# Kernel tuning notes

Measured on AMD Instinct MI355X. Metric: run time of the kernel, lower is better.

## Reference

```python
import jax, jax.numpy as jnp
import numpy as np

B, D_IN, NQ, H = 65536, 385, 64, 16  # batch, input dim, num questions, head width
DIMS = [385, 512, 256, 192]


def setup_inputs() -> dict:
    key = jax.random.key(0)
    ks = jax.random.split(key, 12)
    s = 0.02
    inp = {
        "x": jax.random.normal(ks[0], (B, D_IN), jnp.float32),
        "W1": jax.random.normal(ks[1], (DIMS[0], DIMS[1]), jnp.float32) * s,
        "b1": jnp.zeros((DIMS[1],), jnp.float32),
        "W2": jax.random.normal(ks[2], (DIMS[1], DIMS[2]), jnp.float32) * s,
        "b2": jnp.zeros((DIMS[2],), jnp.float32),
        "W3": jax.random.normal(ks[3], (DIMS[2], DIMS[3]), jnp.float32) * s,
        "b3": jnp.zeros((DIMS[3],), jnp.float32),
        # all true/false heads stacked: layout [qid, correct, H] flattened on last axis
        "Wh": jax.random.normal(ks[4], (DIMS[3], NQ * 2 * H), jnp.float32) * s,
        "bh": jnp.zeros((NQ * 2 * H,), jnp.float32),
        "question_ids": jax.random.randint(ks[5], (B,), 0, NQ, jnp.int32),
        "is_correct": jax.random.randint(ks[6], (B,), 0, 2, jnp.int32),
    }
    return inp


def reference(x, W1, b1, W2, b2, W3, b3, Wh, bh, question_ids, is_correct):
    # shared trunk (dropout is identity at eval); activation = relu
    h = jax.nn.relu(x @ W1 + b1)          # [B, 512]
    h = jax.nn.relu(h @ W2 + b2)          # [B, 256]
    h = jax.nn.relu(h @ W3 + b3)          # [B, 192] shared features
    # compute all heads densely, then gather the per-row head slice —
    # equivalent to routing each row to its (question_id, is_correct) Linear head
    logits_all = h @ Wh + bh              # [B, NQ*2*H]
    base = (question_ids * 2 + is_correct) * H        # [B]
    idx = base[:, None] + jnp.arange(H)[None, :]      # [B, H]
    return jnp.take_along_axis(logits_all, idx, axis=1)  # [B, H]
```

## Files before the change

### kernel.cpp

```cpp
#include <hip/hip_runtime.h>
#include <hip/hip_bf16.h>

#define THREADS 512
#define ROWS 64

typedef __attribute__((ext_vector_type(4))) float f32x4;
typedef __attribute__((ext_vector_type(8))) short s16x8;

__device__ __forceinline__ unsigned short bfbits(float f) {
  __bf16 h = (__bf16)f;
  return __builtin_bit_cast(unsigned short, h);
}
__device__ __forceinline__ float bf2f(unsigned short h) {
  unsigned u = ((unsigned)h) << 16;
  return __builtin_bit_cast(float, u);
}

__global__ void prep_kernel(const float* __restrict__ W1, const float* __restrict__ W2,
                            const float* __restrict__ W3, const float* __restrict__ Wh,
                            unsigned short* __restrict__ w1f, unsigned short* __restrict__ w2f,
                            unsigned short* __restrict__ w3f, unsigned short* __restrict__ whT) {
  int u = blockIdx.x * blockDim.x + threadIdx.x;
  const int U1 = 24576, U2 = 16384, U3 = 6144, U4 = 49152;
  if (u < U1) {
    int lane = u & 63, r = (u >> 6) & 31, c = u >> 11;
    int f  = r * 16 + (lane & 15);
    int kb = c * 32 + ((lane >> 4) << 3);
    s16x8 v;
    #pragma unroll
    for (int j = 0; j < 8; ++j) v[j] = (short)bfbits(W1[(kb + j) * 512 + f]);
    *(s16x8*)(w1f + (u << 3)) = v;
    return;
  }
  u -= U1;
  if (u < U2) {
    int lane = u & 63, r = (u >> 6) & 15, c = u >> 10;
    int f  = r * 16 + (lane & 15);
    int kb = c * 32 + ((lane >> 4) << 3);
    s16x8 v;
    #pragma unroll
    for (int j = 0; j < 8; ++j) v[j] = (short)bfbits(W2[(kb + j) * 256 + f]);
    *(s16x8*)(w2f + (u << 3)) = v;
    return;
  }
  u -= U2;
  if (u < U3) {
    int lane = u & 63, t = u >> 6;
    int c = t / 12, r = t - c * 12;
    int f  = r * 16 + (lane & 15);
    int kb = c * 32 + ((lane >> 4) << 3);
    s16x8 v;
    #pragma unroll
    for (int j = 0; j < 8; ++j) v[j] = (short)bfbits(W3[(kb + j) * 192 + f]);
    *(s16x8*)(w3f + (u << 3)) = v;
    return;
  }
  u -= U3;
  if (u < U4) {
    int j = u & 15, v2 = u >> 4;
    int fo = v2 % 24, head = v2 / 24;
    s16x8 v;
    #pragma unroll
    for (int i = 0; i < 8; ++i) v[i] = (short)bfbits(Wh[(fo * 8 + i) * 2048 + head * 16 + j]);
    *(s16x8*)(whT + u * 8) = v;
  }
}

#define MFMA(a, b, c) __builtin_amdgcn_mfma_f32_16x16x32_bf16((a), (b), (c), 0, 0, 0)
#define SWZ(lp) (((lp) * 16) ^ ((((lp) >> 4) & 3) << 5))

#define G1_RANGE(P, C0, C1)                                                                 \
  _Pragma("unroll")                                                                         \
  for (int c = (C0); c < (C1); ++c) {                                                       \
    s16x8 a0 = *(const s16x8*)(w1f + (((c * 32 + (P) * 16 + w * 2 + 0) * 64 + lane) << 3)); \
    s16x8 a1 = *(const s16x8*)(w1f + (((c * 32 + (P) * 16 + w * 2 + 1) * 64 + lane) << 3)); \
    _Pragma("unroll")                                                                       \
    for (int bt = 0; bt < 4; ++bt) {                                                        \
      s16x8 bfr = *(const s16x8*)(xall + (c << 12) + (bt << 10) + swz_l);                   \
      acc1[0][bt] = MFMA(a0, bfr, acc1[0][bt]);                                             \
      acc1[1][bt] = MFMA(a1, bfr, acc1[1][bt]);                                             \
    }                                                                                       \
  }

__global__ __launch_bounds__(THREADS, 4)
void fused_mlp(const float* __restrict__ x,
               const float* __restrict__ b1,
               const float* __restrict__ b2,
               const float* __restrict__ b3,
               const float* __restrict__ bh,
               const float* __restrict__ W1,
               const int* __restrict__ qid,
               const int* __restrict__ corr,
               const unsigned short* __restrict__ w1f,
               const unsigned short* __restrict__ w2f,
               const unsigned short* __restrict__ w3f,
               const unsigned short* __restrict__ whT,
               float* __restrict__ out) {
  __shared__ __align__(16) unsigned char lds[81920];
  unsigned char*  xall = lds;
  unsigned char*  h1L  = lds;
  unsigned short* h3b  = (unsigned short*)lds;
  unsigned char*  h1H  = lds + 49152;
  unsigned char*  h2f  = lds + 49152;

  const int tid  = threadIdx.x;
  const int lane = tid & 63;
  const int w    = tid >> 6;
  const int b0   = blockIdx.x * ROWS;
  const int l15  = lane & 15;
  const int lh   = lane >> 4;
  const int swz_l = SWZ(lane);

  const int s_ci = tid >> 8;
  const int s_wi = tid & 255;
  const int s_bt = s_wi >> 6;
  const int s_lp = s_wi & 63;
  const float* s_base = x + (size_t)(b0 + (s_bt << 4) + (s_lp & 15)) * 385 + ((s_lp >> 4) << 3);
  const int s_abase = (s_bt << 10) + SWZ(s_lp);

  f32x4 sv0, sv1;
  auto sload = [&](int g) {
    int c = (g << 1) + s_ci;
    sv0 = *(const f32x4*)(s_base + c * 32);
    sv1 = *(const f32x4*)(s_base + c * 32 + 4);
  };
  auto swrite = [&](int g) {
    int c = (g << 1) + s_ci;
    s16x8 v;
    v[0] = (short)bfbits(sv0[0]); v[1] = (short)bfbits(sv0[1]);
    v[2] = (short)bfbits(sv0[2]); v[3] = (short)bfbits(sv0[3]);
    v[4] = (short)bfbits(sv1[0]); v[5] = (short)bfbits(sv1[1]);
    v[6] = (short)bfbits(sv1[2]); v[7] = (short)bfbits(sv1[3]);
    *(s16x8*)(xall + (c << 12) + s_abase) = v;
  };

  f32x4 acc1[2][4];
  #pragma unroll
  for (int a = 0; a < 2; ++a)
    #pragma unroll
    for (int bt = 0; bt < 4; ++bt) acc1[a][bt] = (f32x4)0.0f;

  auto epi1 = [&](int P, unsigned char* dst) {
    #pragma unroll
    for (int a = 0; a < 2; ++a) {
      int ft = w * 2 + a;
      int fg = P * 256 + (ft << 4) + (lh << 2);
      f32x4 bv = *(const f32x4*)(b1 + fg);
      f32x4 wv = *(const f32x4*)(W1 + 384 * 512 + fg);
      int so = ((ft >> 1) << 12) + SWZ(l15 + ((((ft & 1) << 1) + (lh >> 1)) << 4)) + ((lh & 1) << 3);
      #pragma unroll
      for (int bt = 0; bt < 4; ++bt) {
        float xv = x[(size_t)(b0 + (bt << 4) + l15) * 385 + 384];
        float v0 = fmaxf(acc1[a][bt][0] + bv[0] + wv[0] * xv, 0.f);
        float v1 = fmaxf(acc1[a][bt][1] + bv[1] + wv[1] * xv, 0.f);
        float v2 = fmaxf(acc1[a][bt][2] + bv[2] + wv[2] * xv, 0.f);
        float v3 = fmaxf(acc1[a][bt][3] + bv[3] + wv[3] * xv, 0.f);
        unsigned plo = (unsigned)bfbits(v0) | ((unsigned)bfbits(v1) << 16);
        unsigned phi = (unsigned)bfbits(v2) | ((unsigned)bfbits(v3) << 16);
        unsigned long long pk = (unsigned long long)plo | ((unsigned long long)phi << 32);
        *(unsigned long long*)(dst + so + (bt << 10)) = pk;
        acc1[a][bt] = (f32x4)0.0f;
      }
    }
  };

  sload(0); swrite(0);
  __syncthreads();

  sload(1); G1_RANGE(0, 0, 2)  swrite(1); __syncthreads();
  sload(2); G1_RANGE(0, 2, 4)  swrite(2); __syncthreads();
  sload(3); G1_RANGE(0, 4, 6)  swrite(3); __syncthreads();
  sload(4); G1_RANGE(0, 6, 8)  swrite(4); __syncthreads();
  sload(5); G1_RANGE(0, 8, 10) swrite(5); __syncthreads();

  G1_RANGE(0, 10, 12)
  epi1(0, h1H);

  G1_RANGE(1, 0, 12)
  __syncthreads();
  epi1(1, h1L);
  __syncthreads();

  f32x4 acc2[2][4];
  #pragma unroll
  for (int i = 0; i < 2; ++i)
    #pragma unroll
    for (int bt = 0; bt < 4; ++bt) acc2[i][bt] = (f32x4)0.0f;

  #pragma unroll
  for (int c = 0; c < 16; ++c) {
    const unsigned char* reg = (c < 8) ? h1H : h1L;
    int cl = c & 7;
    s16x8 a20 = *(const s16x8*)(w2f + (((c * 16 + w * 2 + 0) * 64 + lane) << 3));
    s16x8 a21 = *(const s16x8*)(w2f + (((c * 16 + w * 2 + 1) * 64 + lane) << 3));
    #pragma unroll
    for (int bt = 0; bt < 4; ++bt) {
      s16x8 bfr = *(const s16x8*)(reg + (cl << 12) + (bt << 10) + swz_l);
      acc2[0][bt] = MFMA(a20, bfr, acc2[0][bt]);
      acc2[1][bt] = MFMA(a21, bfr, acc2[1][bt]);
    }
  }
  __syncthreads();

  #pragma unroll
  for (int i = 0; i < 2; ++i) {
    int ft = w * 2 + i;
    int fg = (ft << 4) + (lh << 2);
    f32x4 bv = *(const f32x4*)(b2 + fg);
    int so = ((ft >> 1) << 12) + SWZ(l15 + ((((ft & 1) << 1) + (lh >> 1)) << 4)) + ((lh & 1) << 3);
    #pragma unroll
    for (int bt = 0; bt < 4; ++bt) {
      float v0 = fmaxf(acc2[i][bt][0] + bv[0], 0.f);
      float v1 = fmaxf(acc2[i][bt][1] + bv[1], 0.f);
      float v2 = fmaxf(acc2[i][bt][2] + bv[2], 0.f);
      float v3 = fmaxf(acc2[i][bt][3] + bv[3], 0.f);
      unsigned plo = (unsigned)bfbits(v0) | ((unsigned)bfbits(v1) << 16);
      unsigned phi = (unsigned)bfbits(v2) | ((unsigned)bfbits(v3) << 16);
      unsigned long long pk = (unsigned long long)plo | ((unsigned long long)phi << 32);
      *(unsigned long long*)(h2f + so + (bt << 10)) = pk;
    }
  }
  __syncthreads();

  const int hrow = tid >> 4, hj = tid & 15;
  const int head0 = qid[b0 + hrow] * 2 + corr[b0 + hrow];
  const int head1 = qid[b0 + 32 + hrow] * 2 + corr[b0 + 32 + hrow];

  {
    f32x4 acc3[2][4];
    #pragma unroll
    for (int i = 0; i < 2; ++i)
      #pragma unroll
      for (int bt = 0; bt < 4; ++bt) acc3[i][bt] = (f32x4)0.0f;

    #pragma unroll
    for (int c = 0; c < 8; ++c) {
      s16x8 a30 = *(const s16x8*)(w3f + (((c * 12 + w) * 64 + lane) << 3));
      s16x8 a31;
      if (w < 4) a31 = *(const s16x8*)(w3f + (((c * 12 + 8 + w) * 64 + lane) << 3));
      #pragma unroll
      for (int bt = 0; bt < 4; ++bt) {
        s16x8 bfr = *(const s16x8*)(h2f + (c << 12) + (bt << 10) + swz_l);
        acc3[0][bt] = MFMA(a30, bfr, acc3[0][bt]);
        if (w < 4) acc3[1][bt] = MFMA(a31, bfr, acc3[1][bt]);
      }
    }
    #pragma unroll
    for (int i = 0; i < 2; ++i) {
      if (i == 0 || w < 4) {
        int ft = (i == 0) ? w : (8 + w);
        int fg = (ft << 4) + (lh << 2);
        f32x4 bv = *(const f32x4*)(b3 + fg);
        #pragma unroll
        for (int bt = 0; bt < 4; ++bt) {
          int row = (bt << 4) + l15;
          float v0 = fmaxf(acc3[i][bt][0] + bv[0], 0.f);
          float v1 = fmaxf(acc3[i][bt][1] + bv[1], 0.f);
          float v2 = fmaxf(acc3[i][bt][2] + bv[2], 0.f);
          float v3 = fmaxf(acc3[i][bt][3] + bv[3], 0.f);
          unsigned plo = (unsigned)bfbits(v0) | ((unsigned)bfbits(v1) << 16);
          unsigned phi = (unsigned)bfbits(v2) | ((unsigned)bfbits(v3) << 16);
          unsigned long long pk = (unsigned long long)plo | ((unsigned long long)phi << 32);
          *(unsigned long long*)((unsigned char*)h3b + row * 400 + (ft << 5) + (lh << 3)) = pk;
        }
      }
    }
  }
  __syncthreads();

  #pragma unroll
  for (int q = 0; q < 2; ++q) {
    int row  = q * 32 + hrow;
    int head = q ? head1 : head0;
    const unsigned short* wp = whT + ((head * 24) * 16 + hj) * 8;
    const unsigned short* hp = h3b + row * 200;
    float acc = bh[(head << 4) + hj];
    #pragma unroll 6
    for (int fo = 0; fo < 24; ++fo) {
      s16x8 wv = *(const s16x8*)(wp + fo * 128);
      s16x8 hv = *(const s16x8*)(hp + fo * 8);
      #pragma unroll
      for (int e = 0; e < 8; ++e)
        acc += bf2f((unsigned short)wv[e]) * bf2f((unsigned short)hv[e]);
    }
    out[(size_t)(b0 + row) * 16 + hj] = acc;
  }
}

extern "C" void kernel_launch(void* const* d_in, const int* in_sizes, int n_in,
                              void* d_out, int out_size, void* d_ws, size_t ws_size,
                              hipStream_t stream) {
  (void)in_sizes; (void)n_in; (void)out_size; (void)ws_size;
  const float* x  = (const float*)d_in[0];
  const float* W1 = (const float*)d_in[1];
  const float* b1 = (const float*)d_in[2];
  const float* W2 = (const float*)d_in[3];
  const float* b2 = (const float*)d_in[4];
  const float* W3 = (const float*)d_in[5];
  const float* b3 = (const float*)d_in[6];
  const float* Wh = (const float*)d_in[7];
  const float* bh = (const float*)d_in[8];
  const int* qid  = (const int*)d_in[9];
  const int* corr = (const int*)d_in[10];
  float* out = (float*)d_out;

  unsigned short* w1f = (unsigned short*)d_ws;
  unsigned short* w2f = w1f + 12 * 32 * 64 * 8;
  unsigned short* w3f = w2f + 16 * 16 * 64 * 8;
  unsigned short* whT = w3f + 8 * 12 * 64 * 8;

  prep_kernel<<<376, 256, 0, stream>>>(W1, W2, W3, Wh, w1f, w2f, w3f, whT);
  fused_mlp<<<65536 / ROWS, THREADS, 0, stream>>>(x, b1, b2, b3, bh, W1, qid, corr,
                                                  w1f, w2f, w3f, whT, out);
}
```

Baseline: 92.43 us.

## Sort rows by head and compute per-head output via MFMA

Adds histogram, prefix-sum and scatter kernels that group batch rows by their (question, correct) head into 16-row-padded segments. The main kernel gathers x rows through this map, so every 16-row tile shares one head and the final head projection becomes a bf16 MFMA instead of a scalar per-thread dot product. The gather replaces the old strided bf16 head loop. In exchange it adds four small launches plus atomics, uncoalesced row gathers of x, and extra padded blocks (1054 instead of 1024).

```diff
diff --git a/kernel.cpp b/kernel.cpp
--- a/kernel.cpp
+++ b/kernel.cpp
@@ -3,6 +3,8 @@
 
 #define THREADS 512
 #define ROWS 64
+#define NPAD 67456
+#define NBLK 1054
 
 typedef __attribute__((ext_vector_type(4))) float f32x4;
 typedef __attribute__((ext_vector_type(8))) short s16x8;
@@ -11,15 +13,11 @@
   __bf16 h = (__bf16)f;
   return __builtin_bit_cast(unsigned short, h);
 }
-__device__ __forceinline__ float bf2f(unsigned short h) {
-  unsigned u = ((unsigned)h) << 16;
-  return __builtin_bit_cast(float, u);
-}
 
 __global__ void prep_kernel(const float* __restrict__ W1, const float* __restrict__ W2,
                             const float* __restrict__ W3, const float* __restrict__ Wh,
                             unsigned short* __restrict__ w1f, unsigned short* __restrict__ w2f,
-                            unsigned short* __restrict__ w3f, unsigned short* __restrict__ whT) {
+                            unsigned short* __restrict__ w3f, unsigned short* __restrict__ whf) {
   int u = blockIdx.x * blockDim.x + threadIdx.x;
   const int U1 = 24576, U2 = 16384, U3 = 6144, U4 = 49152;
   if (u < U1) {
@@ -57,12 +55,48 @@
   }
   u -= U3;
   if (u < U4) {
-    int j = u & 15, v2 = u >> 4;
-    int fo = v2 % 24, head = v2 / 24;
-    s16x8 v;
-    #pragma unroll
-    for (int i = 0; i < 8; ++i) v[i] = (short)bfbits(Wh[(fo * 8 + i) * 2048 + head * 16 + j]);
-    *(s16x8*)(whT + u * 8) = v;
+    int lane = u & 63, t = u >> 6;
+    int c = t % 6, head = t / 6;
+    int kb = c * 32 + ((lane >> 4) << 3);
+    s16x8 v;
+    #pragma unroll
+    for (int j = 0; j < 8; ++j)
+      v[j] = (short)bfbits(Wh[(size_t)(kb + j) * 2048 + head * 16 + (lane & 15)]);
+    *(s16x8*)(whf + (u << 3)) = v;
+  }
+}
+
+__global__ void hist_init_kernel(const int* __restrict__ qid, const int* __restrict__ corr,
+                                 int* __restrict__ cnt, int* __restrict__ rowmap) {
+  int i = blockIdx.x * blockDim.x + threadIdx.x;
+  if (i < NPAD) rowmap[i] = (int)0x80000000;
+  if (i < 65536) atomicAdd(&cnt[qid[i] * 2 + corr[i]], 1);
+}
+
+__global__ void prefix_kernel(const int* __restrict__ cnt, int* __restrict__ cursor) {
+  __shared__ int s[128];
+  int t = threadIdx.x;
+  int padded = (cnt[t] + 15) & ~15;
+  s[t] = padded;
+  __syncthreads();
+  int acc = padded;
+  for (int d = 1; d < 128; d <<= 1) {
+    int v = (t >= d) ? s[t - d] : 0;
+    __syncthreads();
+    acc += v;
+    s[t] = acc;
+    __syncthreads();
+  }
+  cursor[t] = acc - padded;
+}
+
+__global__ void scatter_kernel(const int* __restrict__ qid, const int* __restrict__ corr,
+                               int* __restrict__ cursor, int* __restrict__ rowmap) {
+  int i = blockIdx.x * blockDim.x + threadIdx.x;
+  if (i < 65536) {
+    int h = qid[i] * 2 + corr[i];
+    int pos = atomicAdd(&cursor[h], 1);
+    rowmap[pos] = i;
   }
 }
 
@@ -91,15 +125,16 @@
                const float* __restrict__ W1,
                const int* __restrict__ qid,
                const int* __restrict__ corr,
+               const int* __restrict__ rowmap,
                const unsigned short* __restrict__ w1f,
                const unsigned short* __restrict__ w2f,
                const unsigned short* __restrict__ w3f,
-               const unsigned short* __restrict__ whT,
+               const unsigned short* __restrict__ whf,
                float* __restrict__ out) {
   __shared__ __align__(16) unsigned char lds[81920];
   unsigned char*  xall = lds;
   unsigned char*  h1L  = lds;
-  unsigned short* h3b  = (unsigned short*)lds;
+  unsigned char*  h3f  = lds;
   unsigned char*  h1H  = lds + 49152;
   unsigned char*  h2f  = lds + 49152;
 
@@ -111,11 +146,17 @@
   const int lh   = lane >> 4;
   const int swz_l = SWZ(lane);
 
+  int xro[4];
+  #pragma unroll
+  for (int bt = 0; bt < 4; ++bt)
+    xro[bt] = (rowmap[b0 + (bt << 4) + l15] & 0x7FFFFFFF) * 385;
+
   const int s_ci = tid >> 8;
   const int s_wi = tid & 255;
   const int s_bt = s_wi >> 6;
   const int s_lp = s_wi & 63;
-  const float* s_base = x + (size_t)(b0 + (s_bt << 4) + (s_lp & 15)) * 385 + ((s_lp >> 4) << 3);
+  const int s_xrow = rowmap[b0 + (s_bt << 4) + (s_lp & 15)] & 0x7FFFFFFF;
+  const float* s_base = x + (size_t)s_xrow * 385 + ((s_lp >> 4) << 3);
   const int s_abase = (s_bt << 10) + SWZ(s_lp);
 
   f32x4 sv0, sv1;
@@ -150,7 +191,7 @@
       int so = ((ft >> 1) << 12) + SWZ(l15 + ((((ft & 1) << 1) + (lh >> 1)) << 4)) + ((lh & 1) << 3);
       #pragma unroll
       for (int bt = 0; bt < 4; ++bt) {
-        float xv = x[(size_t)(b0 + (bt << 4) + l15) * 385 + 384];
+        float xv = x[(size_t)xro[bt] + 384];
         float v0 = fmaxf(acc1[a][bt][0] + bv[0] + wv[0] * xv, 0.f);
         float v1 = fmaxf(acc1[a][bt][1] + bv[1] + wv[1] * xv, 0.f);
         float v2 = fmaxf(acc1[a][bt][2] + bv[2] + wv[2] * xv, 0.f);
@@ -222,10 +263,6 @@
   }
   __syncthreads();
 
-  const int hrow = tid >> 4, hj = tid & 15;
-  const int head0 = qid[b0 + hrow] * 2 + corr[b0 + hrow];
-  const int head1 = qid[b0 + 32 + hrow] * 2 + corr[b0 + 32 + hrow];
-
   {
     f32x4 acc3[2][4];
     #pragma unroll
@@ -251,9 +288,9 @@
         int ft = (i == 0) ? w : (8 + w);
         int fg = (ft << 4) + (lh << 2);
         f32x4 bv = *(const f32x4*)(b3 + fg);
+        int so = ((ft >> 1) << 12) + SWZ(l15 + ((((ft & 1) << 1) + (lh >> 1)) << 4)) + ((lh & 1) << 3);
         #pragma unroll
         for (int bt = 0; bt < 4; ++bt) {
-          int row = (bt << 4) + l15;
           float v0 = fmaxf(acc3[i][bt][0] + bv[0], 0.f);
           float v1 = fmaxf(acc3[i][bt][1] + bv[1], 0.f);
           float v2 = fmaxf(acc3[i][bt][2] + bv[2], 0.f);
@@ -261,29 +298,33 @@
           unsigned plo = (unsigned)bfbits(v0) | ((unsigned)bfbits(v1) << 16);
           unsigned phi = (unsigned)bfbits(v2) | ((unsigned)bfbits(v3) << 16);
           unsigned long long pk = (unsigned long long)plo | ((unsigned long long)phi << 32);
-          *(unsigned long long*)((unsigned char*)h3b + row * 400 + (ft << 5) + (lh << 3)) = pk;
+          *(unsigned long long*)(h3f + so + (bt << 10)) = pk;
         }
       }
     }
   }
   __syncthreads();
 
-  #pragma unroll
-  for (int q = 0; q < 2; ++q) {
-    int row  = q * 32 + hrow;
-    int head = q ? head1 : head0;
-    const unsigned short* wp = whT + ((head * 24) * 16 + hj) * 8;
-    const unsigned short* hp = h3b + row * 200;
-    float acc = bh[(head << 4) + hj];
-    #pragma unroll 6
-    for (int fo = 0; fo < 24; ++fo) {
-      s16x8 wv = *(const s16x8*)(wp + fo * 128);
-      s16x8 hv = *(const s16x8*)(hp + fo * 8);
-      #pragma unroll
-      for (int e = 0; e < 8; ++e)
-        acc += bf2f((unsigned short)wv[e]) * bf2f((unsigned short)hv[e]);
-    }
-    out[(size_t)(b0 + row) * 16 + hj] = acc;
+  if (w < 4) {
+    int ts  = b0 + (w << 4);
+    int rm0 = rowmap[ts];
+    int r0  = rm0 & 0x7FFFFFFF;
+    int head = qid[r0] * 2 + corr[r0];
+    f32x4 acch = (f32x4)0.0f;
+    #pragma unroll
+    for (int c = 0; c < 6; ++c) {
+      s16x8 ah  = *(const s16x8*)(whf + (((head * 6 + c) * 64 + lane) << 3));
+      s16x8 bfr = *(const s16x8*)(h3f + (c << 12) + (w << 10) + swz_l);
+      acch = MFMA(ah, bfr, acch);
+    }
+    int rs = rowmap[ts + l15];
+    if (!(rs & 0x80000000)) {
+      f32x4 bv = *(const f32x4*)(bh + (head << 4) + (lh << 2));
+      f32x4 ov;
+      ov[0] = acch[0] + bv[0]; ov[1] = acch[1] + bv[1];
+      ov[2] = acch[2] + bv[2]; ov[3] = acch[3] + bv[3];
+      *(f32x4*)(out + (size_t)rs * 16 + (lh << 2)) = ov;
+    }
   }
 }
 
@@ -305,11 +346,18 @@
   float* out = (float*)d_out;
 
   unsigned short* w1f = (unsigned short*)d_ws;
-  unsigned short* w2f = w1f + 12 * 32 * 64 * 8;
-  unsigned short* w3f = w2f + 16 * 16 * 64 * 8;
-  unsigned short* whT = w3f + 8 * 12 * 64 * 8;
-
-  prep_kernel<<<376, 256, 0, stream>>>(W1, W2, W3, Wh, w1f, w2f, w3f, whT);
-  fused_mlp<<<65536 / ROWS, THREADS, 0, stream>>>(x, b1, b2, b3, bh, W1, qid, corr,
-                                                  w1f, w2f, w3f, whT, out);
-}
+  unsigned short* w2f = w1f + 196608;
+  unsigned short* w3f = w2f + 131072;
+  unsigned short* whf = w3f + 49152;
+  int* cnt    = (int*)(whf + 393216);
+  int* cursor = cnt + 128;
+  int* rowmap = cursor + 128;
+
+  hipMemsetAsync(cnt, 0, 128 * sizeof(int), stream);
+  prep_kernel<<<376, 256, 0, stream>>>(W1, W2, W3, Wh, w1f, w2f, w3f, whf);
+  hist_init_kernel<<<(NPAD + 255) / 256, 256, 0, stream>>>(qid, corr, cnt, rowmap);
+  prefix_kernel<<<1, 128, 0, stream>>>(cnt, cursor);
+  scatter_kernel<<<256, 256, 0, stream>>>(qid, corr, cursor, rowmap);
+  fused_mlp<<<NBLK, THREADS, 0, stream>>>(x, b1, b2, b3, bh, W1, qid, corr, rowmap,
+                                          w1f, w2f, w3f, whf, out);
+}
```

Result: slower. 210.7 us (+127.9%).
